# Kernel optimization log

Measured on AMD Instinct MI355X. Metric: run time of the kernel, lower is better.

The kernel has to match this reference:

```python
import jax, jax.numpy as jnp
import numpy as np

B, L, HSIZE = 16, 512, 1024
H, D = 16, 64  # HHEAD = HSIZE/base, HBASE = 64

def setup_inputs() -> dict:
    key = jax.random.key(0)
    ks = jax.random.split(key, 10)
    inp = {
        'v': jax.random.normal(ks[0], (B, L, HSIZE), jnp.float32),
        'k': jax.random.normal(ks[1], (B, L, HSIZE), jnp.float32),
        'q': jax.random.normal(ks[2], (B, L, HSIZE), jnp.float32),
        'img_abs': jax.random.normal(ks[3], (B, L, HSIZE), jnp.float32),
        'Wv': jax.random.normal(ks[4], (HSIZE, HSIZE), jnp.float32) * 0.02,
        'Wk': jax.random.normal(ks[5], (HSIZE, HSIZE), jnp.float32) * 0.02,
        'Wq': jax.random.normal(ks[6], (HSIZE, HSIZE), jnp.float32) * 0.02,
        'Wm': jax.random.normal(ks[7], (HSIZE, HSIZE), jnp.float32) * 0.02,
        'abs_mask': jax.random.bernoulli(ks[8], 0.1, (B, 1, L, L)),
        'mask': jax.random.bernoulli(ks[9], 0.1, (B, 1, L, L)),
    }
    return inp

def reference(v, k, q, img_abs, Wv, Wk, Wq, Wm, abs_mask, mask):
    nb = q.shape[0]
    # Linear (no bias) then split heads: [B, L, HSIZE] -> [B, H, L, D]
    def heads(x):
        return x.reshape(nb, -1, H, D).transpose(0, 2, 1, 3)
    vh = heads(v @ Wv.T)
    kh = heads(k @ Wk.T)
    qh = heads(q @ Wq.T)
    ph = heads(img_abs)
    scale = 1.0 / jnp.sqrt(jnp.asarray(D, qh.dtype))
    # modulate: attention of q over positional features, residual-added to q
    s1 = jnp.einsum('bhqd,bhpd->bhqp', qh, ph) * scale
    s1 = jnp.where(abs_mask, jnp.asarray(-1e9, s1.dtype), s1)
    qh = qh + jnp.einsum('bhqp,bhpd->bhqd', jax.nn.softmax(s1, axis=-1), ph)
    # main attention (dropout = identity in eval mode)
    s2 = jnp.einsum('bhqd,bhkd->bhqk', qh, kh) * scale
    s2 = jnp.where(mask, jnp.asarray(-1e9, s2.dtype), s2)
    atted = jnp.einsum('bhqk,bhkd->bhqd', jax.nn.softmax(s2, axis=-1), vh)
    atted = atted.transpose(0, 2, 1, 3).reshape(nb, -1, H * D)
    return atted @ Wm.T
```

## Files before the change

kernel.cpp:

```cpp
#include <hip/hip_runtime.h>

typedef unsigned short u16;
typedef unsigned int u32;
typedef unsigned long long u64;
typedef __attribute__((ext_vector_type(8))) short short8;
typedef __attribute__((ext_vector_type(4))) float f32x4;

#define NB 16
#define SL 512
#define HS 1024
#define NHEAD 16
#define HD 64
#define NTOKC (16L * 512 * 1024)
#define NWC   (1024L * 1024)
#define NMC   (16L * 512 * 512)

typedef const __attribute__((address_space(1))) u32* gas_t;
typedef __attribute__((address_space(3))) u32* las_t;

__device__ __forceinline__ void gld16(const u16* g, u16* l) {
  __builtin_amdgcn_global_load_lds((gas_t)g, (las_t)l, 16, 0, 0);
}

__device__ __forceinline__ u16 f2bf(float f) {
  union { float f; unsigned u; } c; c.f = f;
  unsigned r = c.u + 0x7FFFu + ((c.u >> 16) & 1u);
  return (u16)(r >> 16);
}
__device__ __forceinline__ float bf2f(u16 u) {
  union { float f; unsigned u; } c; c.u = ((unsigned)u) << 16;
  return c.f;
}

__global__ __launch_bounds__(256) void prep(
    const float* __restrict__ v, const float* __restrict__ k,
    const float* __restrict__ q, const float* __restrict__ img,
    const float* __restrict__ Wv, const float* __restrict__ Wk,
    const float* __restrict__ Wq, const float* __restrict__ Wm,
    const int* __restrict__ absm, const int* __restrict__ mask,
    u16* __restrict__ ovk, u16* __restrict__ xq, u16* __restrict__ pb,
    u16* __restrict__ w4, u64* __restrict__ bits) {
  const int y = blockIdx.y;
  const long bx = blockIdx.x;
  if (y < 4) {
    const float* in = y == 0 ? v : y == 1 ? k : y == 2 ? q : img;
    u16* out = y == 0 ? ovk : y == 1 ? ovk + NTOKC : y == 2 ? xq : pb;
    long i = (bx * 256 + threadIdx.x) * 4;
    float4 f = *(const float4*)(in + i);
    uint2 u;
    u.x = (unsigned)f2bf(f.x) | ((unsigned)f2bf(f.y) << 16);
    u.y = (unsigned)f2bf(f.z) | ((unsigned)f2bf(f.w) << 16);
    *(uint2*)(out + i) = u;
  } else if (y == 4) {
    if (bx >= 4096) return;
    long i = bx * 1024 + threadIdx.x * 4;
    int j = (int)(i >> 20);
    const float* in = j == 0 ? Wv : j == 1 ? Wk : j == 2 ? Wq : Wm;
    long off = i & (NWC - 1);
    float4 f = *(const float4*)(in + off);
    uint2 u;
    u.x = (unsigned)f2bf(f.x) | ((unsigned)f2bf(f.y) << 16);
    u.y = (unsigned)f2bf(f.z) | ((unsigned)f2bf(f.w) << 16);
    *(uint2*)(w4 + i) = u;
  } else {
#pragma unroll
    for (int rep = 0; rep < 4; ++rep) {
      long i = (bx * 4 + rep) * 256 + threadIdx.x;
      const int* m = (i >= NMC) ? mask : absm;
      long off = i & (NMC - 1);
      u64 bset = __ballot(m[off] != 0);
      if ((threadIdx.x & 63) == 0) bits[i >> 6] = bset;
    }
  }
}

__global__ __launch_bounds__(256) void gemm_p3(const u16* __restrict__ Avk,
                                               const u16* __restrict__ Aq,
                                               const u16* __restrict__ W4,
                                               u16* __restrict__ Cb) {
  __shared__ u16 As[128 * 64];
  __shared__ u16 Bs[128 * 64];
  const int tid = threadIdx.x;
  const int wave = tid >> 6, lane = tid & 63;
  const int quad = lane >> 4, l16 = lane & 15;
  const int l7 = l16 & 7;
  const int sel = blockIdx.x >> 6;
  const int row0 = (blockIdx.x & 63) * 128, col0 = blockIdx.y * 128;
  const int wm = (wave >> 1) * 64, wn = (wave & 1) * 64;
  const int lrow = lane >> 3;
  const int scb = (lane & 7) ^ lrow;
  const int K = HS, N = HS;

  const u16* A = (sel == 2) ? Aq : Avk + (long)sel * NTOKC;
  const u16* W = W4 + (long)sel * NWC;
  u16* C = Cb + (long)sel * NTOKC;

  f32x4 acc[4][4];
#pragma unroll
  for (int mt = 0; mt < 4; ++mt)
#pragma unroll
    for (int nt = 0; nt < 4; ++nt) acc[mt][nt] = (f32x4){0.f, 0.f, 0.f, 0.f};

  const u16* Ab = A + (long)row0 * K;
  const u16* Wb = W + (long)col0 * K;

  for (int k0 = 0; k0 < K; k0 += 64) {
    __syncthreads();
#pragma unroll
    for (int it = 0; it < 4; ++it) {
      int seg = wave * 4 + it;
      int r = seg * 8 + lrow;
      gld16(Ab + (long)r * K + k0 + scb * 8, As + seg * 512);
      gld16(Wb + (long)r * K + k0 + scb * 8, Bs + seg * 512);
    }
    __syncthreads();
#pragma unroll
    for (int kt = 0; kt < 2; ++kt) {
      short8 af[4], bw[4];
#pragma unroll
      for (int mt = 0; mt < 4; ++mt)
        af[mt] = *(const short8*)(As + (wm + mt * 16 + l16) * 64 +
                                  (((kt * 4 + quad) ^ l7) * 8));
#pragma unroll
      for (int nt = 0; nt < 4; ++nt)
        bw[nt] = *(const short8*)(Bs + (wn + nt * 16 + l16) * 64 +
                                  (((kt * 4 + quad) ^ l7) * 8));
#pragma unroll
      for (int mt = 0; mt < 4; ++mt)
#pragma unroll
        for (int nt = 0; nt < 4; ++nt)
          acc[mt][nt] = __builtin_amdgcn_mfma_f32_16x16x32_bf16(
              af[mt], bw[nt], acc[mt][nt], 0, 0, 0);
    }
  }
#pragma unroll
  for (int mt = 0; mt < 4; ++mt)
#pragma unroll
    for (int nt = 0; nt < 4; ++nt)
#pragma unroll
      for (int i = 0; i < 4; ++i) {
        long r = row0 + wm + mt * 16 + quad * 4 + i;
        long c = col0 + wn + nt * 16 + l16;
        C[r * N + c] = f2bf(acc[mt][nt][i]);
      }
}

__global__ __launch_bounds__(256, 4) void gemm_f(const u16* __restrict__ A,
                                                 const u16* __restrict__ W,
                                                 float* __restrict__ C) {
  __shared__ u16 As[64 * 64];
  __shared__ u16 Bs[128 * 64];
  const int tid = threadIdx.x;
  const int wave = tid >> 6, lane = tid & 63;
  const int quad = lane >> 4, l16 = lane & 15;
  const int l7 = l16 & 7;
  const int row0 = blockIdx.x * 64, col0 = blockIdx.y * 128;
  const int wm = (wave >> 1) * 32, wn = (wave & 1) * 64;
  const int lrow = lane >> 3;
  const int scb = (lane & 7) ^ lrow;
  const int K = HS, N = HS;

  f32x4 acc[2][4];
#pragma unroll
  for (int mt = 0; mt < 2; ++mt)
#pragma unroll
    for (int nt = 0; nt < 4; ++nt) acc[mt][nt] = (f32x4){0.f, 0.f, 0.f, 0.f};

  const u16* Ab = A + (long)row0 * K;
  const u16* Wb = W + (long)col0 * K;

  for (int k0 = 0; k0 < K; k0 += 64) {
    __syncthreads();
#pragma unroll
    for (int it = 0; it < 2; ++it) {
      int seg = wave * 2 + it;
      gld16(Ab + (long)(seg * 8 + lrow) * K + k0 + scb * 8, As + seg * 512);
    }
#pragma unroll
    for (int it = 0; it < 4; ++it) {
      int seg = wave * 4 + it;
      gld16(Wb + (long)(seg * 8 + lrow) * K + k0 + scb * 8, Bs + seg * 512);
    }
    __syncthreads();
#pragma unroll
    for (int kt = 0; kt < 2; ++kt) {
      short8 af[2], bw[4];
#pragma unroll
      for (int mt = 0; mt < 2; ++mt)
        af[mt] = *(const short8*)(As + (wm + mt * 16 + l16) * 64 +
                                  (((kt * 4 + quad) ^ l7) * 8));
#pragma unroll
      for (int nt = 0; nt < 4; ++nt)
        bw[nt] = *(const short8*)(Bs + (wn + nt * 16 + l16) * 64 +
                                  (((kt * 4 + quad) ^ l7) * 8));
#pragma unroll
      for (int mt = 0; mt < 2; ++mt)
#pragma unroll
        for (int nt = 0; nt < 4; ++nt)
          acc[mt][nt] = __builtin_amdgcn_mfma_f32_16x16x32_bf16(
              af[mt], bw[nt], acc[mt][nt], 0, 0, 0);
    }
  }
#pragma unroll
  for (int mt = 0; mt < 2; ++mt)
#pragma unroll
    for (int nt = 0; nt < 4; ++nt)
#pragma unroll
      for (int i = 0; i < 4; ++i) {
        long r = row0 + wm + mt * 16 + quad * 4 + i;
        long c = col0 + wn + nt * 16 + l16;
        C[r * N + c] = acc[mt][nt][i];
      }
}

__device__ __forceinline__ void attn_stage(
    const u16* __restrict__ Kb, const u16* __restrict__ Vb,
    const u32* __restrict__ Mb, int q0, short8 qf[2], float l_i[4],
    f32x4 o[4], u16 (*Ks)[72], u16 (*Vs)[72], u16 (*Ps)[72],
    int wave, int quad, int l16, int sr, int sds, int vcol) {
  uint4 kp0 = *(const uint4*)(Kb + (long)sr * HS + sds);
  uint4 kp1 = *(const uint4*)(Kb + (long)sr * HS + sds + 8);
  uint4 vp0 = *(const uint4*)(Vb + (long)sr * HS + sds);
  uint4 vp1 = *(const uint4*)(Vb + (long)sr * HS + sds + 8);
  for (int t = 0; t < 8; ++t) {
    __syncthreads();
    *(uint4*)&Ks[sr][sds] = kp0;
    *(uint4*)&Ks[sr][sds + 8] = kp1;
    {
      union { uint4 q[2]; u16 e[16]; } tv;
      tv.q[0] = vp0; tv.q[1] = vp1;
#pragma unroll
      for (int j = 0; j < 16; ++j) Vs[sds + j][vcol] = tv.e[j];
    }
    __syncthreads();
    if (t < 7) {
      const u16* Kn = Kb + (long)((t + 1) * 64 + sr) * HS;
      kp0 = *(const uint4*)(Kn + sds);
      kp1 = *(const uint4*)(Kn + sds + 8);
      const u16* Vn = Vb + (long)((t + 1) * 64 + sr) * HS;
      vp0 = *(const uint4*)(Vn + sds);
      vp1 = *(const uint4*)(Vn + sds + 8);
    }
    f32x4 s[4];
#pragma unroll
    for (int nt = 0; nt < 4; ++nt) s[nt] = (f32x4){0.f, 0.f, 0.f, 0.f};
#pragma unroll
    for (int kt = 0; kt < 2; ++kt)
#pragma unroll
      for (int nt = 0; nt < 4; ++nt) {
        short8 bk = *(const short8*)&Ks[nt * 16 + l16][kt * 32 + quad * 8];
        s[nt] = __builtin_amdgcn_mfma_f32_16x16x32_bf16(qf[kt], bk, s[nt], 0, 0, 0);
      }
#pragma unroll
    for (int i = 0; i < 4; ++i) {
      int gr = q0 + wave * 16 + quad * 4 + i;
      uint2 mw = *(const uint2*)&Mb[(long)gr * 16 + t * 2];
#pragma unroll
      for (int nt = 0; nt < 4; ++nt) {
        u32 w = (nt & 2) ? mw.y : mw.x;
        int msk = (w >> ((nt & 1) * 16 + l16)) & 1;
        float p = msk ? 0.f : __expf(s[nt][i] * 0.125f);
        l_i[i] += p;
        Ps[wave * 16 + quad * 4 + i][nt * 16 + l16] = f2bf(p);
      }
    }
#pragma unroll
    for (int kt = 0; kt < 2; ++kt) {
      short8 ap = *(const short8*)&Ps[wave * 16 + l16][kt * 32 + quad * 8];
#pragma unroll
      for (int nt = 0; nt < 4; ++nt) {
        short8 bv = *(const short8*)&Vs[nt * 16 + l16]
                                      [(kt * 32 + quad * 8) ^ ((nt & 3) << 4)];
        o[nt] = __builtin_amdgcn_mfma_f32_16x16x32_bf16(ap, bv, o[nt], 0, 0, 0);
      }
    }
  }
}

__global__ __launch_bounds__(256) void attn_fused(
    const u16* __restrict__ Qp, const u16* __restrict__ Pbp,
    const u16* __restrict__ Kp, const u16* __restrict__ Vp,
    const u32* __restrict__ B0, const u32* __restrict__ B1,
    u16* __restrict__ Op) {
  __shared__ u16 Ks[64][72];
  __shared__ u16 Vs[64][72];
  __shared__ u16 Ps[64][72];
  const int tid = threadIdx.x;
  const int wave = tid >> 6, lane = tid & 63;
  const int quad = lane >> 4, l16 = lane & 15;
  const int qt = blockIdx.x, h = blockIdx.y, b = blockIdx.z;
  const int q0 = qt * 64;
  const long bs = (long)SL * HS;
  const u16* Qb = Qp + (long)b * bs + h * HD;
  const u16* Pb = Pbp + (long)b * bs + h * HD;
  const u16* Kb = Kp + (long)b * bs + h * HD;
  const u16* Vb = Vp + (long)b * bs + h * HD;
  const u32* M0 = B0 + (long)b * SL * 16;
  const u32* M1 = B1 + (long)b * SL * 16;
  const int sr = tid >> 2, sds = (tid & 3) * 16;
  const int vcol = sr ^ (((sds >> 4) & 3) << 4);

  short8 qf[2];
#pragma unroll
  for (int kt = 0; kt < 2; ++kt)
    qf[kt] = *(const short8*)(Qb + (long)(q0 + wave * 16 + l16) * HS +
                              kt * 32 + quad * 8);

  float l_i[4] = {0.f, 0.f, 0.f, 0.f};
  f32x4 o[4];
#pragma unroll
  for (int nt = 0; nt < 4; ++nt) o[nt] = (f32x4){0.f, 0.f, 0.f, 0.f};

  attn_stage(Pb, Pb, M0, q0, qf, l_i, o, Ks, Vs, Ps, wave, quad, l16, sr, sds, vcol);

#pragma unroll
  for (int i = 0; i < 4; ++i) {
    float rs = l_i[i];
#pragma unroll
    for (int off = 8; off >= 1; off >>= 1) rs += __shfl_xor(rs, off, 64);
    float inv = 1.f / rs;
#pragma unroll
    for (int nt = 0; nt < 4; ++nt)
      Ps[wave * 16 + quad * 4 + i][nt * 16 + l16] = f2bf(o[nt][i] * inv);
    l_i[i] = 0.f;
  }
#pragma unroll
  for (int kt = 0; kt < 2; ++kt) {
    short8 t8 = *(const short8*)&Ps[wave * 16 + l16][kt * 32 + quad * 8];
#pragma unroll
    for (int j = 0; j < 8; ++j)
      qf[kt][j] = (short)f2bf(bf2f((u16)t8[j]) + bf2f((u16)qf[kt][j]));
  }
#pragma unroll
  for (int nt = 0; nt < 4; ++nt) o[nt] = (f32x4){0.f, 0.f, 0.f, 0.f};

  attn_stage(Kb, Vb, M1, q0, qf, l_i, o, Ks, Vs, Ps, wave, quad, l16, sr, sds, vcol);

  u16* Ob = Op + (long)b * bs + h * HD;
#pragma unroll
  for (int i = 0; i < 4; ++i) {
    float rs = l_i[i];
#pragma unroll
    for (int off = 8; off >= 1; off >>= 1) rs += __shfl_xor(rs, off, 64);
    float inv = 1.f / rs;
    int r = q0 + wave * 16 + quad * 4 + i;
#pragma unroll
    for (int nt = 0; nt < 4; ++nt)
      Ob[(long)r * HS + nt * 16 + l16] = f2bf(o[nt][i] * inv);
  }
}

extern "C" void kernel_launch(void* const* d_in, const int* in_sizes, int n_in,
                              void* d_out, int out_size, void* d_ws,
                              size_t ws_size, hipStream_t stream) {
  const float* v   = (const float*)d_in[0];
  const float* k   = (const float*)d_in[1];
  const float* q   = (const float*)d_in[2];
  const float* img = (const float*)d_in[3];
  const float* Wv  = (const float*)d_in[4];
  const float* Wk  = (const float*)d_in[5];
  const float* Wq  = (const float*)d_in[6];
  const float* Wm  = (const float*)d_in[7];
  const int* absm  = (const int*)d_in[8];
  const int* mask  = (const int*)d_in[9];
  float* out = (float*)d_out;

  const long NTOK = NTOKC;
  const long NW   = NWC;
  const long NM   = NMC;
  u16* ovk = (u16*)d_out;
  u16* ws  = (u16*)d_ws;
  u16* xq  = ws;
  u16* pb  = ws + 1 * NTOK;
  u16* vh  = ws + 2 * NTOK;
  u16* kh  = ws + 3 * NTOK;
  u16* qh  = ws + 4 * NTOK;
  u16* w4  = ws + 5 * NTOK;
  u64* bt0 = (u64*)(w4 + 4 * NW);
  u64* bt1 = bt0 + NM / 64;
  u16* att = xq;

  prep<<<dim3(8192, 6), 256, 0, stream>>>(v, k, q, img, Wv, Wk, Wq, Wm,
                                          absm, mask, ovk, xq, pb, w4, bt0);
  gemm_p3<<<dim3(192, 8), 256, 0, stream>>>(ovk, xq, w4, vh);
  attn_fused<<<dim3(SL / 64, NHEAD, NB), 256, 0, stream>>>(
      qh, pb, kh, vh, (const u32*)bt0, (const u32*)bt1, att);
  gemm_f<<<dim3(NB * SL / 64, HS / 128), 256, 0, stream>>>(att, w4 + 3 * NW, out);
}
```

Baseline: 395.2 us.

## Enlarge attention query tile to 128 rows and gemm_f tile to 128x128

The attention kernel now uses 512-thread blocks covering 128 query rows, so each staged K/V tile is shared by twice as many queries. Each thread loads 8 elements instead of 16, and the first stage loads the shared P tile once, reusing it for both K and V. The output GEMM moves to 128x128 tiles with 4x4 MFMA accumulators per wave to raise operand reuse. The cost is fewer blocks in the grid and higher register and LDS use per block, which may lower occupancy.

```diff
diff --git a/kernel.cpp b/kernel.cpp
--- a/kernel.cpp
+++ b/kernel.cpp
@@ -145,24 +145,24 @@
       }
 }
 
-__global__ __launch_bounds__(256, 4) void gemm_f(const u16* __restrict__ A,
-                                                 const u16* __restrict__ W,
-                                                 float* __restrict__ C) {
-  __shared__ u16 As[64 * 64];
+__global__ __launch_bounds__(256) void gemm_f(const u16* __restrict__ A,
+                                              const u16* __restrict__ W,
+                                              float* __restrict__ C) {
+  __shared__ u16 As[128 * 64];
   __shared__ u16 Bs[128 * 64];
   const int tid = threadIdx.x;
   const int wave = tid >> 6, lane = tid & 63;
   const int quad = lane >> 4, l16 = lane & 15;
   const int l7 = l16 & 7;
-  const int row0 = blockIdx.x * 64, col0 = blockIdx.y * 128;
-  const int wm = (wave >> 1) * 32, wn = (wave & 1) * 64;
+  const int row0 = blockIdx.x * 128, col0 = blockIdx.y * 128;
+  const int wm = (wave >> 1) * 64, wn = (wave & 1) * 64;
   const int lrow = lane >> 3;
   const int scb = (lane & 7) ^ lrow;
   const int K = HS, N = HS;
 
-  f32x4 acc[2][4];
-#pragma unroll
-  for (int mt = 0; mt < 2; ++mt)
+  f32x4 acc[4][4];
+#pragma unroll
+  for (int mt = 0; mt < 4; ++mt)
 #pragma unroll
     for (int nt = 0; nt < 4; ++nt) acc[mt][nt] = (f32x4){0.f, 0.f, 0.f, 0.f};
 
@@ -172,21 +172,18 @@
   for (int k0 = 0; k0 < K; k0 += 64) {
     __syncthreads();
 #pragma unroll
-    for (int it = 0; it < 2; ++it) {
-      int seg = wave * 2 + it;
-      gld16(Ab + (long)(seg * 8 + lrow) * K + k0 + scb * 8, As + seg * 512);
-    }
-#pragma unroll
     for (int it = 0; it < 4; ++it) {
       int seg = wave * 4 + it;
-      gld16(Wb + (long)(seg * 8 + lrow) * K + k0 + scb * 8, Bs + seg * 512);
+      int r = seg * 8 + lrow;
+      gld16(Ab + (long)r * K + k0 + scb * 8, As + seg * 512);
+      gld16(Wb + (long)r * K + k0 + scb * 8, Bs + seg * 512);
     }
     __syncthreads();
 #pragma unroll
     for (int kt = 0; kt < 2; ++kt) {
-      short8 af[2], bw[4];
-#pragma unroll
-      for (int mt = 0; mt < 2; ++mt)
+      short8 af[4], bw[4];
+#pragma unroll
+      for (int mt = 0; mt < 4; ++mt)
         af[mt] = *(const short8*)(As + (wm + mt * 16 + l16) * 64 +
                                   (((kt * 4 + quad) ^ l7) * 8));
 #pragma unroll
@@ -194,7 +191,7 @@
         bw[nt] = *(const short8*)(Bs + (wn + nt * 16 + l16) * 64 +
                                   (((kt * 4 + quad) ^ l7) * 8));
 #pragma unroll
-      for (int mt = 0; mt < 2; ++mt)
+      for (int mt = 0; mt < 4; ++mt)
 #pragma unroll
         for (int nt = 0; nt < 4; ++nt)
           acc[mt][nt] = __builtin_amdgcn_mfma_f32_16x16x32_bf16(
@@ -202,7 +199,7 @@
     }
   }
 #pragma unroll
-  for (int mt = 0; mt < 2; ++mt)
+  for (int mt = 0; mt < 4; ++mt)
 #pragma unroll
     for (int nt = 0; nt < 4; ++nt)
 #pragma unroll
@@ -213,33 +210,28 @@
       }
 }
 
+template <bool SAME>
 __device__ __forceinline__ void attn_stage(
     const u16* __restrict__ Kb, const u16* __restrict__ Vb,
     const u32* __restrict__ Mb, int q0, short8 qf[2], float l_i[4],
-    f32x4 o[4], u16 (*Ks)[72], u16 (*Vs)[72], u16 (*Ps)[72],
+    f32x4 o[4], u16 (*Ks)[72], u16 (*Vs)[72], u16 (*Ps)[76],
     int wave, int quad, int l16, int sr, int sds, int vcol) {
-  uint4 kp0 = *(const uint4*)(Kb + (long)sr * HS + sds);
-  uint4 kp1 = *(const uint4*)(Kb + (long)sr * HS + sds + 8);
-  uint4 vp0 = *(const uint4*)(Vb + (long)sr * HS + sds);
-  uint4 vp1 = *(const uint4*)(Vb + (long)sr * HS + sds + 8);
+  uint4 kp = *(const uint4*)(Kb + (long)sr * HS + sds);
+  uint4 vp = SAME ? kp : *(const uint4*)(Vb + (long)sr * HS + sds);
   for (int t = 0; t < 8; ++t) {
     __syncthreads();
-    *(uint4*)&Ks[sr][sds] = kp0;
-    *(uint4*)&Ks[sr][sds + 8] = kp1;
+    *(uint4*)&Ks[sr][sds] = kp;
     {
-      union { uint4 q[2]; u16 e[16]; } tv;
-      tv.q[0] = vp0; tv.q[1] = vp1;
-#pragma unroll
-      for (int j = 0; j < 16; ++j) Vs[sds + j][vcol] = tv.e[j];
+      union { uint4 q; u16 e[8]; } tv;
+      tv.q = SAME ? kp : vp;
+#pragma unroll
+      for (int j = 0; j < 8; ++j) Vs[sds + j][vcol] = tv.e[j];
     }
     __syncthreads();
     if (t < 7) {
-      const u16* Kn = Kb + (long)((t + 1) * 64 + sr) * HS;
-      kp0 = *(const uint4*)(Kn + sds);
-      kp1 = *(const uint4*)(Kn + sds + 8);
-      const u16* Vn = Vb + (long)((t + 1) * 64 + sr) * HS;
-      vp0 = *(const uint4*)(Vn + sds);
-      vp1 = *(const uint4*)(Vn + sds + 8);
+      kp = *(const uint4*)(Kb + (long)((t + 1) * 64 + sr) * HS + sds);
+      if (!SAME)
+        vp = *(const uint4*)(Vb + (long)((t + 1) * 64 + sr) * HS + sds);
     }
     f32x4 s[4];
 #pragma unroll
@@ -277,19 +269,19 @@
   }
 }
 
-__global__ __launch_bounds__(256) void attn_fused(
+__global__ __launch_bounds__(512, 8) void attn_fused(
     const u16* __restrict__ Qp, const u16* __restrict__ Pbp,
     const u16* __restrict__ Kp, const u16* __restrict__ Vp,
     const u32* __restrict__ B0, const u32* __restrict__ B1,
     u16* __restrict__ Op) {
   __shared__ u16 Ks[64][72];
   __shared__ u16 Vs[64][72];
-  __shared__ u16 Ps[64][72];
+  __shared__ u16 Ps[128][76];
   const int tid = threadIdx.x;
   const int wave = tid >> 6, lane = tid & 63;
   const int quad = lane >> 4, l16 = lane & 15;
   const int qt = blockIdx.x, h = blockIdx.y, b = blockIdx.z;
-  const int q0 = qt * 64;
+  const int q0 = qt * 128;
   const long bs = (long)SL * HS;
   const u16* Qb = Qp + (long)b * bs + h * HD;
   const u16* Pb = Pbp + (long)b * bs + h * HD;
@@ -297,7 +289,7 @@
   const u16* Vb = Vp + (long)b * bs + h * HD;
   const u32* M0 = B0 + (long)b * SL * 16;
   const u32* M1 = B1 + (long)b * SL * 16;
-  const int sr = tid >> 2, sds = (tid & 3) * 16;
+  const int sr = tid >> 3, sds = (tid & 7) * 8;
   const int vcol = sr ^ (((sds >> 4) & 3) << 4);
 
   short8 qf[2];
@@ -311,7 +303,8 @@
 #pragma unroll
   for (int nt = 0; nt < 4; ++nt) o[nt] = (f32x4){0.f, 0.f, 0.f, 0.f};
 
-  attn_stage(Pb, Pb, M0, q0, qf, l_i, o, Ks, Vs, Ps, wave, quad, l16, sr, sds, vcol);
+  attn_stage<true>(Pb, Pb, M0, q0, qf, l_i, o, Ks, Vs, Ps, wave, quad, l16,
+                   sr, sds, vcol);
 
 #pragma unroll
   for (int i = 0; i < 4; ++i) {
@@ -334,7 +327,8 @@
 #pragma unroll
   for (int nt = 0; nt < 4; ++nt) o[nt] = (f32x4){0.f, 0.f, 0.f, 0.f};
 
-  attn_stage(Kb, Vb, M1, q0, qf, l_i, o, Ks, Vs, Ps, wave, quad, l16, sr, sds, vcol);
+  attn_stage<false>(Kb, Vb, M1, q0, qf, l_i, o, Ks, Vs, Ps, wave, quad, l16,
+                    sr, sds, vcol);
 
   u16* Ob = Op + (long)b * bs + h * HD;
 #pragma unroll
@@ -383,7 +377,8 @@
   prep<<<dim3(8192, 6), 256, 0, stream>>>(v, k, q, img, Wv, Wk, Wq, Wm,
                                           absm, mask, ovk, xq, pb, w4, bt0);
   gemm_p3<<<dim3(192, 8), 256, 0, stream>>>(ovk, xq, w4, vh);
-  attn_fused<<<dim3(SL / 64, NHEAD, NB), 256, 0, stream>>>(
+  attn_fused<<<dim3(SL / 128, NHEAD, NB), 512, 0, stream>>>(
       qh, pb, kh, vh, (const u32*)bt0, (const u32*)bt1, att);
-  gemm_f<<<dim3(NB * SL / 64, HS / 128), 256, 0, stream>>>(att, w4 + 3 * NW, out);
-}
+  gemm_f<<<dim3(NB * SL / 128, HS / 128), 256, 0, stream>>>(att, w4 + 3 * NW,
+                                                            out);
+}
```

Measured after the change: 472.7 us. 1.2x slower.
